# Performance work log

Hardware: AMD Instinct MI355X
Metric: run time of the kernel (lower is better)

Reference implementation:

```python
import jax, jax.numpy as jnp
import numpy as np

# Irreps config: node = 64x0e + 32x1o, edge sh = 1x0e + 1x1o
N, E = 50000, 800000
MUL0, MUL1 = 64, 32
D_IN = MUL0 + 3 * MUL1          # 160
FC_H = 64
W_NUMEL = MUL0 + MUL0 + MUL1 + MUL1  # 192, per-instruction uvu weights
SQRT3 = 1.7320508075688772
ACT_C = 1.6791   # e3nn normalize2mom constant for silu


def setup_inputs() -> dict:
    key = jax.random.key(0)
    ks = jax.random.split(key, 11)
    return {
        "x": jax.random.normal(ks[0], (N, D_IN), jnp.float32),
        "edge_scalars": jax.random.uniform(ks[1], (E, FC_H), dtype=jnp.float32),
        "edge_attr_sh": jax.random.normal(ks[2], (E, 4), jnp.float32),
        "edge_index": jax.random.randint(ks[3], (2, E), 0, N),
        "w_fc1": jax.random.normal(ks[4], (FC_H, FC_H), jnp.float32),
        "w_fc2": jax.random.normal(ks[5], (FC_H, W_NUMEL), jnp.float32),
        "w_sc_s": jax.random.normal(ks[6], (MUL0, MUL0), jnp.float32),
        "w_sc_v": jax.random.normal(ks[7], (MUL1, MUL1), jnp.float32),
        "w_lin_s": jax.random.normal(ks[8], (96, MUL0), jnp.float32),
        "w_lin_v": jax.random.normal(ks[9], (96, MUL1), jnp.float32),
        "w_alpha": jax.random.normal(ks[10], (96, 1), jnp.float32) * 0.1,
    }


def reference(x, edge_scalars, edge_attr_sh, edge_index, w_fc1, w_fc2,
              w_sc_s, w_sc_v, w_lin_s, w_lin_v, w_alpha):
    src, dst = edge_index[0], edge_index[1]

    # --- fc: FullyConnectedNet([64, 64, 192], silu), e3nn fan-in norm ---
    h = jax.nn.silu(edge_scalars @ w_fc1 / np.sqrt(FC_H)) * ACT_C
    weight = h @ w_fc2 / np.sqrt(FC_H)                       # [E, 192]
    w0 = weight[:, :MUL0]                 # 0e x 0e -> 0e (mul 64)
    w1 = weight[:, MUL0:2 * MUL0]         # 0e x 1o -> 1o (mul 64)
    w2 = weight[:, 2 * MUL0:2 * MUL0 + MUL1]   # 1o x 0e -> 1o (mul 32)
    w3 = weight[:, 2 * MUL0 + MUL1:]           # 1o x 1o -> 0e (mul 32)

    # --- self connection: o3.Linear(in -> out), per-irrep mixing ---
    x_s = x[:, :MUL0]                                   # [N, 64]
    x_v = x[:, MUL0:].reshape(N, MUL1, 3)               # [N, 32, 3]
    sc_s = x_s @ w_sc_s / np.sqrt(MUL0)
    sc_v = jnp.einsum('nui,uw->nwi', x_v, w_sc_v) / np.sqrt(MUL1)
    sc_out = jnp.concatenate([sc_s, sc_v.reshape(N, 3 * MUL1)], axis=1)

    # --- gather + edge-weighted uvu tensor product ---
    gx_s = x_s[src]                                     # [E, 64]
    gx_v = x_v[src]                                     # [E, 32, 3]
    sh_s = edge_attr_sh[:, 0:1]                         # [E, 1]
    sh_v = edge_attr_sh[:, 1:4]                         # [E, 3]

    # path weights fold with w3j so factors cancel for 1o outputs
    mid_s0 = w0 * gx_s * sh_s                                        # [E,64] 0e
    mid_s1 = w3 * jnp.einsum('eui,ei->eu', gx_v, sh_v) / SQRT3       # [E,32] 0e
    mid_v0 = w1[:, :, None] * gx_s[:, :, None] * sh_v[:, None, :]    # [E,64,3] 1o
    mid_v1 = w2[:, :, None] * gx_v * sh_s[:, :, None]                # [E,32,3] 1o
    edge_feat = jnp.concatenate(
        [mid_s0, mid_s1, mid_v0.reshape(E, 3 * MUL0), mid_v1.reshape(E, 3 * MUL1)],
        axis=1)                                                      # [E, 384]

    # --- scatter-mean to destination nodes ---
    seg = jax.ops.segment_sum(edge_feat, dst, num_segments=N)
    cnt = jax.ops.segment_sum(jnp.ones((E,), edge_feat.dtype), dst, num_segments=N)
    mean = seg / jnp.maximum(cnt, 1.0)[:, None]                      # [N, 384]

    m_s = mean[:, :96]                                   # 96x0e
    m_v = mean[:, 96:].reshape(N, 96, 3)                 # 96x1o

    # --- alpha gate (o3.Linear mid -> 0e) and output linear ---
    alpha = m_s @ w_alpha / np.sqrt(96)                  # [N, 1]
    lin_s = m_s @ w_lin_s / np.sqrt(96)                  # [N, 64]
    lin_v = jnp.einsum('nui,uw->nwi', m_v, w_lin_v) / np.sqrt(96)
    lin_out = jnp.concatenate([lin_s, lin_v.reshape(N, 3 * MUL1)], axis=1)

    # sc.output_mask is all-ones here (every output irrep reachable)
    return sc_out + alpha * lin_out
```

## Files before the change

### kernel.cpp

```cpp
#include <hip/hip_runtime.h>
#include <hip/hip_bf16.h>

#define N_NODES 50000
#define N_EDGES 800000
#define MUL0 64
#define MUL1 32
#define D_IN 160
#define FC_H 64
#define W_NUMEL 192
#define FEAT 384
#define ACT_C 1.6791f
#define INV_SQRT3 0.57735026918962576f
#define RSQRT32 0.17677669529663687f
#define RSQRT96 0.10206207261596575f

#define TILE 64

typedef __attribute__((ext_vector_type(8))) short s16x8;
typedef __attribute__((ext_vector_type(4))) float f32x4;
typedef _Float16 h8 __attribute__((ext_vector_type(8)));
typedef __fp16 fp16x2 __attribute__((ext_vector_type(2)));

static __device__ __forceinline__ unsigned short f2bf(float f) {
    __hip_bfloat16 b = __float2bfloat16(f);
    return __builtin_bit_cast(unsigned short, b);
}

static __device__ __forceinline__ int swz(int row, int byte_in_row) {
    return row * 128 + ((((byte_in_row >> 4) ^ (row & 7)) << 4) | (byte_in_row & 15));
}
static __device__ __forceinline__ h8 rdh8(const unsigned char* base, int row, int eb) {
    return *(const h8*)(base + swz(row, eb));
}


__global__ __launch_bounds__(256) void hist_kernel(const int* __restrict__ eidx,
                                                   int* __restrict__ cnt) {
    int e = blockIdx.x * 256 + threadIdx.x;
    if (e < N_EDGES) atomicAdd(&cnt[eidx[N_EDGES + e]], 1);
}

#define SCAN_NB 64
#define SCAN_CH ((N_NODES + SCAN_NB - 1) / SCAN_NB)

__global__ __launch_bounds__(256) void scanA_kernel(const int* __restrict__ cnt,
                                                    int* __restrict__ bsum) {
    __shared__ int sred[4];
    int b = blockIdx.x, t = threadIdx.x;
    int lim = min((b + 1) * SCAN_CH, N_NODES);
    int s = 0;
    for (int i = b * SCAN_CH + t; i < lim; i += 256) s += cnt[i];
    for (int d = 1; d < 64; d <<= 1) s += __shfl_xor(s, d);
    if ((t & 63) == 0) sred[t >> 6] = s;
    __syncthreads();
    if (t == 0) bsum[b] = sred[0] + sred[1] + sred[2] + sred[3];
}

__global__ __launch_bounds__(64) void scanB_kernel(const int* __restrict__ bsum,
                                                   int* __restrict__ boff) {
    int t = threadIdx.x;
    int v = bsum[t];
    int p = v;
    for (int d = 1; d < 64; d <<= 1) { int u = __shfl_up(p, d); if (t >= d) p += u; }
    boff[t] = p - v;
}

__global__ __launch_bounds__(256) void scanC_kernel(const int* __restrict__ cnt,
                                                    const int* __restrict__ boff,
                                                    int* __restrict__ fill) {
    __shared__ int s_w[4];
    int b = blockIdx.x, t = threadIdx.x;
    const int CH2 = (SCAN_CH + 255) / 256;
    int base = b * SCAN_CH + t * CH2;
    int lim = min((b + 1) * SCAN_CH, N_NODES);
    int s = 0;
#pragma unroll
    for (int k = 0; k < CH2; ++k) { int i = base + k; if (i < lim) s += cnt[i]; }
    int v = s;
    for (int d = 1; d < 64; d <<= 1) { int u = __shfl_up(v, d); if ((t & 63) >= d) v += u; }
    if ((t & 63) == 63) s_w[t >> 6] = v;
    __syncthreads();
    if (t == 0) { int run = 0; for (int w = 0; w < 4; ++w) { int tv = s_w[w]; s_w[w] = run; run += tv; } }
    __syncthreads();
    int run = boff[b] + s_w[t >> 6] + (v - s);
#pragma unroll
    for (int k = 0; k < CH2; ++k) {
        int i = base + k;
        if (i < lim) { fill[i] = run; run += cnt[i]; }
    }
}

__global__ __launch_bounds__(256) void scatter_ids_kernel(const int* __restrict__ eidx,
                                                          int* __restrict__ fill,
                                                          int* __restrict__ sorted_eid) {
    int e = blockIdx.x * 256 + threadIdx.x;
    if (e < N_EDGES) {
        int p = atomicAdd(&fill[eidx[N_EDGES + e]], 1);
        sorted_eid[p] = e;
    }
}

__global__ __launch_bounds__(256) void prep_w_kernel(
    const float* __restrict__ w_fc1,
    const float* __restrict__ w_fc2,
    const float* __restrict__ w_sc_s,
    const float* __restrict__ w_sc_v,
    const float* __restrict__ w_lin_s,
    const float* __restrict__ w_lin_v,
    unsigned short* __restrict__ w1t,
    unsigned short* __restrict__ w2t,
    unsigned short* __restrict__ wscs_t,
    unsigned short* __restrict__ wscv_t,
    unsigned short* __restrict__ wlins_t,
    unsigned short* __restrict__ wlinv_t)
{
    int i = blockIdx.x * 256 + threadIdx.x;
    if (i < 64 * 64)  w1t[i]    = f2bf(w_fc1[(i & 63) * FC_H + (i >> 6)]);
    if (i < 192 * 64) w2t[i]    = f2bf(w_fc2[(i & 63) * W_NUMEL + (i >> 6)]);
    if (i < 64 * 64)  wscs_t[i] = f2bf(w_sc_s[(i & 63) * 64 + (i >> 6)]);
    if (i < 32 * 32)  wscv_t[i] = f2bf(w_sc_v[(i & 31) * 32 + (i >> 5)]);
    if (i < 64 * 96)  wlins_t[i] = f2bf(w_lin_s[(i % 96) * 64 + (i / 96)]);
    if (i < 32 * 96)  wlinv_t[i] = f2bf(w_lin_v[(i % 96) * 32 + (i / 96)]);
}

#define X_OFF    0
#define W_OFF    20480
#define SH_OFF   45056
#define SID_OFF  45568
#define SEGN_OFF 45696
#define NSEG_OFF 45952
#define SMEM_SZ  45968

static __device__ __forceinline__ h8 seg_mask(const unsigned* vv, unsigned tgt) {
    h8 a;
#pragma unroll
    for (int w2 = 0; w2 < 4; ++w2) {
        a[w2 * 2]     = ((vv[w2] & 0xffffu) == tgt) ? (_Float16)1.f : (_Float16)0.f;
        a[w2 * 2 + 1] = ((vv[w2] >> 16)     == tgt) ? (_Float16)1.f : (_Float16)0.f;
    }
    return a;
}

__global__ __launch_bounds__(256) void edge_kernel(
    const float* __restrict__ x,
    const float* __restrict__ es,
    const float* __restrict__ sh,
    const int*   __restrict__ eidx,
    const int*   __restrict__ sorted_eid,
    const unsigned short* __restrict__ w1t,
    const unsigned short* __restrict__ w2t,
    float* __restrict__ accg)
{
    __shared__ __align__(16) unsigned char smem[SMEM_SZ];
    int* s_segnode = (int*)(smem + SEGN_OFF);
    unsigned short* s_sid = (unsigned short*)(smem + SID_OFF);

    const int t = threadIdx.x;
    const int l = t & 63;
    const int wv = t >> 6;
    const int lr = l & 15;
    const int lk = l >> 4;
    const int tile0 = blockIdx.x * TILE;

    int eid_own = sorted_eid[tile0 + wv * 16 + lr];
    float4 esf[4];
    {
        const float4* ep = (const float4*)(es + (size_t)eid_own * FC_H);
        esf[0] = ep[lk * 2];     esf[1] = ep[lk * 2 + 1];
        esf[2] = ep[8 + lk * 2]; esf[3] = ep[8 + lk * 2 + 1];
    }
    float4 xg[10];
    int xE[10], xC[10];
#pragma unroll
    for (int q = 0; q < 10; ++q) {
        int i = q * 256 + t;
        int e = i / 40, c4 = i - e * 40;
        xE[q] = e; xC[q] = c4;
        const float4* xp = (const float4*)(x + (size_t)eidx[sorted_eid[tile0 + e]] * D_IN);
        xg[q] = xp[c4];
    }
    float shv = sh[(size_t)sorted_eid[tile0 + (t >> 2)] * 4 + (t & 3)];
    if (wv == 0) {
        int dl = eidx[N_EDGES + sorted_eid[tile0 + l]];
        int nd = __shfl_down(dl, 1);
        bool flag = (l == 63) || (dl != nd);
        unsigned long long m = __ballot(flag);
        int sid = __popcll(m & ((1ull << l) - 1ull));
        s_sid[l] = (unsigned short)sid;
        if (flag) s_segnode[sid] = dl;
        if (l == 63) *(int*)(smem + NSEG_OFF) = sid + 1;
    }

    unsigned short* s_h = (unsigned short*)(smem + X_OFF);
    s16x8 afrag[2];
    {
        s16x8 a;
        a[0] = f2bf(esf[0].x); a[1] = f2bf(esf[0].y); a[2] = f2bf(esf[0].z); a[3] = f2bf(esf[0].w);
        a[4] = f2bf(esf[1].x); a[5] = f2bf(esf[1].y); a[6] = f2bf(esf[1].z); a[7] = f2bf(esf[1].w);
        afrag[0] = a;
        a[0] = f2bf(esf[2].x); a[1] = f2bf(esf[2].y); a[2] = f2bf(esf[2].z); a[3] = f2bf(esf[2].w);
        a[4] = f2bf(esf[3].x); a[5] = f2bf(esf[3].y); a[6] = f2bf(esf[3].z); a[7] = f2bf(esf[3].w);
        afrag[1] = a;
    }
#pragma unroll
    for (int nt = 0; nt < 4; ++nt) {
        f32x4 hacc = {0.f, 0.f, 0.f, 0.f};
#pragma unroll
        for (int kk = 0; kk < 2; ++kk) {
            s16x8 b = *(const s16x8*)(w1t + (nt * 16 + lr) * 64 + kk * 32 + lk * 8);
            hacc = __builtin_amdgcn_mfma_f32_16x16x32_bf16(afrag[kk], b, hacc, 0, 0, 0);
        }
#pragma unroll
        for (int q = 0; q < 4; ++q) {
            float aa = hacc[q] * 0.125f;
            float hv = aa * (1.f / (1.f + __expf(-aa))) * ACT_C;
            s_h[(wv * 16 + lk * 4 + q) * 72 + nt * 16 + lr] = f2bf(hv);
        }
    }
    s16x8 hfrag[2];
#pragma unroll
    for (int kk = 0; kk < 2; ++kk)
        hfrag[kk] = *(const s16x8*)(s_h + (wv * 16 + lr) * 72 + kk * 32 + lk * 8);
    __syncthreads();

#pragma unroll
    for (int nt = 0; nt < 12; ++nt) {
        f32x4 acc = {0.f, 0.f, 0.f, 0.f};
#pragma unroll
        for (int kk = 0; kk < 2; ++kk) {
            s16x8 b = *(const s16x8*)(w2t + (nt * 16 + lr) * 64 + kk * 32 + lk * 8);
            acc = __builtin_amdgcn_mfma_f32_16x16x32_bf16(hfrag[kk], b, acc, 0, 0, 0);
        }
        int f = nt * 16 + lr;
        fp16x2 p0 = __builtin_amdgcn_cvt_pkrtz(acc[0] * 0.125f, acc[1] * 0.125f);
        fp16x2 p1 = __builtin_amdgcn_cvt_pkrtz(acc[2] * 0.125f, acc[3] * 0.125f);
        uint2 wval = { __builtin_bit_cast(unsigned, p0), __builtin_bit_cast(unsigned, p1) };
        *(uint2*)(smem + W_OFF + swz(f, wv * 32 + lk * 8)) = wval;
    }
#pragma unroll
    for (int q = 0; q < 10; ++q) {
        float4 v = xg[q];
#pragma unroll
        for (int jj = 0; jj < 4; ++jj) {
            int r = xC[q] * 4 + jj;
            float fv = (jj == 0) ? v.x : (jj == 1) ? v.y : (jj == 2) ? v.z : v.w;
            *(_Float16*)(smem + X_OFF + swz(r, xE[q] * 2)) = (_Float16)fv;
        }
    }
    {
        int e = t >> 2, c = t & 3;
        *(_Float16*)(smem + SH_OFF + swz(c, e * 2)) = (_Float16)shv;
    }
    __syncthreads();

    const int nseg = *(const int*)(smem + NSEG_OFF);

    h8 shreg[4][2];
#pragma unroll
    for (int r = 0; r < 4; ++r)
#pragma unroll
        for (int ks = 0; ks < 2; ++ks)
            shreg[r][ks] = rdh8(smem + SH_OFF, r, ks * 64 + lk * 16);
    unsigned vv[2][4];
#pragma unroll
    for (int ks = 0; ks < 2; ++ks) {
        uint4 sv = *(const uint4*)(smem + SID_OFF + ks * 64 + lk * 16);
        vv[ks][0] = sv.x; vv[ks][1] = sv.y; vv[ks][2] = sv.z; vv[ks][3] = sv.w;
    }

    h8 Bv[4][2];
    int fcol[4];
    bool cls3j[4] = {false, false, false, false};
#pragma unroll
    for (int ks = 0; ks < 2; ++ks) {
        const int eb = ks * 64 + lk * 16;
        if (wv == 0) {
#pragma unroll
            for (int jj = 0; jj < 4; ++jj) {
                int col = jj * 16 + lr;
                Bv[jj][ks] = rdh8(smem + W_OFF, col, eb) * rdh8(smem + X_OFF, col, eb);
                fcol[jj] = col;
            }
        } else if (wv == 1) {
#pragma unroll
            for (int jj = 0; jj < 4; ++jj) {
                int col = jj * 16 + lr;
                Bv[jj][ks] = rdh8(smem + W_OFF, 128 + col / 3, eb) * rdh8(smem + X_OFF, 64 + col, eb);
                fcol[jj] = 288 + col;
            }
        } else if (wv == 2) {
#pragma unroll
            for (int jj = 0; jj < 2; ++jj) {
                int col = 64 + jj * 16 + lr;
                Bv[jj][ks] = rdh8(smem + W_OFF, 128 + col / 3, eb) * rdh8(smem + X_OFF, 64 + col, eb);
                fcol[jj] = 288 + col;
            }
#pragma unroll
            for (int jj = 2; jj < 4; ++jj) {
                int col = (jj - 2) * 16 + lr;
                h8 d = rdh8(smem + X_OFF, 64 + 3 * col, eb)     * shreg[1][ks]
                     + rdh8(smem + X_OFF, 64 + 3 * col + 1, eb) * shreg[2][ks]
                     + rdh8(smem + X_OFF, 64 + 3 * col + 2, eb) * shreg[3][ks];
                Bv[jj][ks] = rdh8(smem + W_OFF, 160 + col, eb) * d;
                fcol[jj] = 64 + col;
                cls3j[jj] = true;
            }
        } else {
#pragma unroll
            for (int jj = 0; jj < 4; ++jj) {
                int col = jj * 16 + lr;
                Bv[jj][ks] = rdh8(smem + W_OFF, 64 + col, eb) * rdh8(smem + X_OFF, col, eb);
                fcol[jj] = 96 + 3 * col;
            }
        }
    }

    if (wv != 3) {
        const int npass = (nseg + 15) >> 4;
        for (int p = 0; p < npass; ++p) {
            h8 bm0 = seg_mask(vv[0], (unsigned)(p * 16 + lr));
            h8 bm1 = seg_mask(vv[1], (unsigned)(p * 16 + lr));
            h8 As0 = bm0 * shreg[0][0];
            h8 As1 = bm1 * shreg[0][1];
            const int m0 = p * 16 + lk * 4;
            float* nptr[4]; bool valid[4], atq[4];
#pragma unroll
            for (int q = 0; q < 4; ++q) {
                int sg = m0 + q;
                valid[q] = sg < nseg;
                int node = valid[q] ? s_segnode[sg] : 0;
                nptr[q] = accg + (size_t)node * FEAT;
                atq[q] = (sg == 0) || (sg == nseg - 1);
            }
#pragma unroll
            for (int jj = 0; jj < 4; ++jj) {
                f32x4 acc = {0.f, 0.f, 0.f, 0.f};
                acc = __builtin_amdgcn_mfma_f32_16x16x32_f16(cls3j[jj] ? bm0 : As0, Bv[jj][0], acc, 0, 0, 0);
                acc = __builtin_amdgcn_mfma_f32_16x16x32_f16(cls3j[jj] ? bm1 : As1, Bv[jj][1], acc, 0, 0, 0);
                const float sc = cls3j[jj] ? INV_SQRT3 : 1.f;
#pragma unroll
                for (int q = 0; q < 4; ++q) {
                    if (valid[q]) {
                        float v = acc[q] * sc;
                        float* a = nptr[q] + fcol[jj];
                        if (atq[q]) atomicAdd(a, v); else *a = v;
                    }
                }
            }
        }
    } else {
        const int npass = (3 * nseg + 15) >> 4;
        for (int p = 0; p < npass; ++p) {
            int m = p * 16 + lr;
            int sgA = m / 3, i3A = m - 3 * sgA;
            h8 mk0 = seg_mask(vv[0], (unsigned)sgA);
            h8 mk1 = seg_mask(vv[1], (unsigned)sgA);
            h8 A0 = mk0 * ((i3A == 0) ? shreg[1][0] : (i3A == 1) ? shreg[2][0] : shreg[3][0]);
            h8 A1 = mk1 * ((i3A == 0) ? shreg[1][1] : (i3A == 1) ? shreg[2][1] : shreg[3][1]);
            int m0 = p * 16 + lk * 4;
            int sgq = m0 / 3, rq = m0 - 3 * sgq;
            float* nptr[4]; int i3q[4]; bool valid[4], atq[4];
#pragma unroll
            for (int q = 0; q < 4; ++q) {
                valid[q] = sgq < nseg;
                int node = valid[q] ? s_segnode[sgq] : 0;
                nptr[q] = accg + (size_t)node * FEAT;
                i3q[q] = rq;
                atq[q] = (sgq == 0) || (sgq == nseg - 1);
                if (++rq == 3) { rq = 0; ++sgq; }
            }
#pragma unroll
            for (int jj = 0; jj < 4; ++jj) {
                f32x4 acc = {0.f, 0.f, 0.f, 0.f};
                acc = __builtin_amdgcn_mfma_f32_16x16x32_f16(A0, Bv[jj][0], acc, 0, 0, 0);
                acc = __builtin_amdgcn_mfma_f32_16x16x32_f16(A1, Bv[jj][1], acc, 0, 0, 0);
#pragma unroll
                for (int q = 0; q < 4; ++q) {
                    if (valid[q]) {
                        float* a = nptr[q] + fcol[jj] + i3q[q];
                        if (atq[q]) atomicAdd(a, acc[q]); else *a = acc[q];
                    }
                }
            }
        }
    }
}


static __device__ __forceinline__ s16x8 frag_c8(const float* p, float s) {
    float4 u = *(const float4*)p, v = *(const float4*)(p + 4);
    s16x8 a;
    a[0] = f2bf(u.x * s); a[1] = f2bf(u.y * s); a[2] = f2bf(u.z * s); a[3] = f2bf(u.w * s);
    a[4] = f2bf(v.x * s); a[5] = f2bf(v.y * s); a[6] = f2bf(v.z * s); a[7] = f2bf(v.w * s);
    return a;
}

__global__ __launch_bounds__(256) void node_kernel(
    const float* __restrict__ x,
    const float* __restrict__ accg,
    const int*   __restrict__ cnt,
    const unsigned short* __restrict__ wscs_t,
    const unsigned short* __restrict__ wscv_t,
    const unsigned short* __restrict__ wlins_t,
    const unsigned short* __restrict__ wlinv_t,
    const float* __restrict__ w_alpha,
    float* __restrict__ out)
{
    const int t = threadIdx.x;
    const int wv = t >> 6, l = t & 63;
    const int lr = l & 15, lk = l >> 4;
    const int n_base = blockIdx.x * 64 + wv * 16;
    const int nrow = n_base + lr;
    const int nclamp = min(nrow, N_NODES - 1);

    const float* mrow = accg + (size_t)nclamp * FEAT;
    const float* xrow = x + (size_t)nclamp * D_IN;
    const float rinv = 1.f / (float)max(cnt[nclamp], 1);

    s16x8 ax[2], ams[3], axv[3], amv[3][3];
#pragma unroll
    for (int kk = 0; kk < 2; ++kk) ax[kk] = frag_c8(xrow + kk * 32 + lk * 8, 1.f);
#pragma unroll
    for (int kk = 0; kk < 3; ++kk) ams[kk] = frag_c8(mrow + kk * 32 + lk * 8, rinv);
    {
        float xb[24];
        const float4* p = (const float4*)(xrow + 64 + 24 * lk);
#pragma unroll
        for (int q = 0; q < 6; ++q) ((float4*)xb)[q] = p[q];
#pragma unroll
        for (int i = 0; i < 3; ++i) {
            s16x8 a;
#pragma unroll
            for (int j = 0; j < 8; ++j) a[j] = f2bf(xb[3 * j + i]);
            axv[i] = a;
        }
    }
#pragma unroll
    for (int kk = 0; kk < 3; ++kk) {
        float mb[24];
        const float4* p = (const float4*)(mrow + 96 + 96 * kk + 24 * lk);
#pragma unroll
        for (int q = 0; q < 6; ++q) ((float4*)mb)[q] = p[q];
#pragma unroll
        for (int i = 0; i < 3; ++i) {
            s16x8 a;
#pragma unroll
            for (int j = 0; j < 8; ++j) a[j] = f2bf(mb[3 * j + i] * rinv);
            amv[i][kk] = a;
        }
    }

    float ap = 0.f;
    {
        float ab[24];
        const float4* p = (const float4*)(mrow + 24 * lk);
#pragma unroll
        for (int q = 0; q < 6; ++q) ((float4*)ab)[q] = p[q];
#pragma unroll
        for (int j = 0; j < 24; ++j) ap += ab[j] * rinv * w_alpha[lk * 24 + j];
    }
    ap += __shfl_xor(ap, 16);
    ap += __shfl_xor(ap, 32);
    const float alphav = ap * RSQRT96;

    f32x4 accA[4], accL[4];
#pragma unroll
    for (int nt = 0; nt < 4; ++nt) { accA[nt] = (f32x4){0,0,0,0}; accL[nt] = (f32x4){0,0,0,0}; }
#pragma unroll
    for (int nt = 0; nt < 4; ++nt) {
#pragma unroll
        for (int kk = 0; kk < 2; ++kk) {
            s16x8 b = *(const s16x8*)(wscs_t + (nt * 16 + lr) * 64 + kk * 32 + lk * 8);
            accA[nt] = __builtin_amdgcn_mfma_f32_16x16x32_bf16(ax[kk], b, accA[nt], 0, 0, 0);
        }
#pragma unroll
        for (int kk = 0; kk < 3; ++kk) {
            s16x8 b = *(const s16x8*)(wlins_t + (nt * 16 + lr) * 96 + kk * 32 + lk * 8);
            accL[nt] = __builtin_amdgcn_mfma_f32_16x16x32_bf16(ams[kk], b, accL[nt], 0, 0, 0);
        }
    }
    f32x4 accVs[3][2], accVl[3][2];
#pragma unroll
    for (int i = 0; i < 3; ++i)
#pragma unroll
        for (int nt = 0; nt < 2; ++nt) { accVs[i][nt] = (f32x4){0,0,0,0}; accVl[i][nt] = (f32x4){0,0,0,0}; }
#pragma unroll
    for (int i = 0; i < 3; ++i) {
#pragma unroll
        for (int nt = 0; nt < 2; ++nt) {
            s16x8 b = *(const s16x8*)(wscv_t + (nt * 16 + lr) * 32 + lk * 8);
            accVs[i][nt] = __builtin_amdgcn_mfma_f32_16x16x32_bf16(axv[i], b, accVs[i][nt], 0, 0, 0);
#pragma unroll
            for (int kk = 0; kk < 3; ++kk) {
                s16x8 b2 = *(const s16x8*)(wlinv_t + (nt * 16 + lr) * 96 + kk * 32 + lk * 8);
                accVl[i][nt] = __builtin_amdgcn_mfma_f32_16x16x32_bf16(amv[i][kk], b2, accVl[i][nt], 0, 0, 0);
            }
        }
    }

#pragma unroll
    for (int q = 0; q < 4; ++q) {
        int row = lk * 4 + q;
        float ar = __shfl(alphav, row);
        int n = n_base + row;
        bool ok = (n < N_NODES);
        float* orow = out + (size_t)n * 160;
#pragma unroll
        for (int nt = 0; nt < 4; ++nt) {
            float vout = accA[nt][q] * 0.125f + ar * accL[nt][q] * RSQRT96;
            if (ok) orow[nt * 16 + lr] = vout;
        }
#pragma unroll
        for (int i = 0; i < 3; ++i)
#pragma unroll
            for (int nt = 0; nt < 2; ++nt) {
                float vout = accVs[i][nt][q] * RSQRT32 + ar * accVl[i][nt][q] * RSQRT96;
                if (ok) orow[64 + 3 * (nt * 16 + lr) + i] = vout;
            }
    }
}


extern "C" void kernel_launch(void* const* d_in, const int* in_sizes, int n_in,
                              void* d_out, int out_size, void* d_ws, size_t ws_size,
                              hipStream_t stream) {
    const float* x        = (const float*)d_in[0];
    const float* es       = (const float*)d_in[1];
    const float* sh       = (const float*)d_in[2];
    const int*   eidx     = (const int*)d_in[3];
    const float* w_fc1    = (const float*)d_in[4];
    const float* w_fc2    = (const float*)d_in[5];
    const float* w_sc_s   = (const float*)d_in[6];
    const float* w_sc_v   = (const float*)d_in[7];
    const float* w_lin_s  = (const float*)d_in[8];
    const float* w_lin_v  = (const float*)d_in[9];
    const float* w_alpha  = (const float*)d_in[10];
    float* out = (float*)d_out;

    float* accg       = (float*)d_ws;
    int*   cnt        = (int*)(accg + (size_t)N_NODES * FEAT);
    int*   fill       = cnt + N_NODES;
    int*   sorted_eid = fill + N_NODES;
    unsigned short* w1t     = (unsigned short*)(sorted_eid + N_EDGES);
    unsigned short* w2t     = w1t + 64 * 64;
    unsigned short* wscs_t  = w2t + 192 * 64;
    unsigned short* wscv_t  = wscs_t + 64 * 64;
    unsigned short* wlins_t = wscv_t + 32 * 32;
    unsigned short* wlinv_t = wlins_t + 64 * 96;
    int* bsum = (int*)(wlinv_t + 32 * 96);
    int* boff = bsum + SCAN_NB;

    (void)hipMemsetAsync(d_ws, 0, ((size_t)N_NODES * FEAT + N_NODES) * 4, stream);
    hipLaunchKernelGGL(hist_kernel, dim3((N_EDGES + 255) / 256), dim3(256), 0, stream,
                       eidx, cnt);
    hipLaunchKernelGGL(scanA_kernel, dim3(SCAN_NB), dim3(256), 0, stream, cnt, bsum);
    hipLaunchKernelGGL(scanB_kernel, dim3(1), dim3(64), 0, stream, bsum, boff);
    hipLaunchKernelGGL(scanC_kernel, dim3(SCAN_NB), dim3(256), 0, stream, cnt, boff, fill);
    hipLaunchKernelGGL(scatter_ids_kernel, dim3((N_EDGES + 255) / 256), dim3(256), 0, stream,
                       eidx, fill, sorted_eid);
    hipLaunchKernelGGL(prep_w_kernel, dim3(48), dim3(256), 0, stream,
                       w_fc1, w_fc2, w_sc_s, w_sc_v, w_lin_s, w_lin_v,
                       w1t, w2t, wscs_t, wscv_t, wlins_t, wlinv_t);
    hipLaunchKernelGGL(edge_kernel, dim3(N_EDGES / TILE), dim3(256), 0, stream,
                       x, es, sh, eidx, sorted_eid, w1t, w2t, accg);
    hipLaunchKernelGGL(node_kernel, dim3((N_NODES + 63) / 64), dim3(256), 0, stream,
                       x, accg, cnt, wscs_t, wscv_t, wlins_t, wlinv_t, w_alpha, out);
}
```

Measured before the change: 453.0 us.

## Split shared-memory tiles into per-half-edge slabs and coalesce node-feature gathers

Changes the swizzle so each 128-byte row holds two logical 64-byte rows, and splits the W, X and SH shared buffers into two slabs, one per 32-edge half. The node-feature gather changes so each thread loads ten contiguous float4s of a single source node instead of striding across edges, which removes the per-element div/mod indexing. The goal is better global coalescing per node row and fewer LDS bank conflicts on the half-precision transposed writes. It risks layout mismatches with the unseen consumers of these buffers, and it may raise register pressure.

```diff
diff --git a/kernel.cpp b/kernel.cpp
--- a/kernel.cpp
+++ b/kernel.cpp
@@ -27,7 +27,9 @@
 }
 
 static __device__ __forceinline__ int swz(int row, int byte_in_row) {
-    return row * 128 + ((((byte_in_row >> 4) ^ (row & 7)) << 4) | (byte_in_row & 15));
+    int unit = ((row & 1) << 2) | (byte_in_row >> 4);
+    int su = unit ^ ((row >> 1) & 7);
+    return (row >> 1) * 128 + su * 16 + (byte_in_row & 15);
 }
 static __device__ __forceinline__ h8 rdh8(const unsigned char* base, int row, int eb) {
     return *(const h8*)(base + swz(row, eb));
@@ -169,15 +171,15 @@
         esf[0] = ep[lk * 2];     esf[1] = ep[lk * 2 + 1];
         esf[2] = ep[8 + lk * 2]; esf[3] = ep[8 + lk * 2 + 1];
     }
+    const int hs   = t >> 7;
+    const int tt_h = t & 127;
+    const int xe   = tt_h & 31;
+    const int cgrp = tt_h >> 5;
     float4 xg[10];
-    int xE[10], xC[10];
-#pragma unroll
-    for (int q = 0; q < 10; ++q) {
-        int i = q * 256 + t;
-        int e = i / 40, c4 = i - e * 40;
-        xE[q] = e; xC[q] = c4;
-        const float4* xp = (const float4*)(x + (size_t)eidx[sorted_eid[tile0 + e]] * D_IN);
-        xg[q] = xp[c4];
+    {
+        const float4* xp = (const float4*)(x + (size_t)eidx[sorted_eid[tile0 + hs * 32 + xe]] * D_IN);
+#pragma unroll
+        for (int k = 0; k < 10; ++k) xg[k] = xp[cgrp * 10 + k];
     }
     float shv = sh[(size_t)sorted_eid[tile0 + (t >> 2)] * 4 + (t & 3)];
     if (wv == 0) {
@@ -223,47 +225,54 @@
         hfrag[kk] = *(const s16x8*)(s_h + (wv * 16 + lr) * 72 + kk * 32 + lk * 8);
     __syncthreads();
 
-#pragma unroll
-    for (int nt = 0; nt < 12; ++nt) {
-        f32x4 acc = {0.f, 0.f, 0.f, 0.f};
-#pragma unroll
-        for (int kk = 0; kk < 2; ++kk) {
-            s16x8 b = *(const s16x8*)(w2t + (nt * 16 + lr) * 64 + kk * 32 + lk * 8);
-            acc = __builtin_amdgcn_mfma_f32_16x16x32_bf16(hfrag[kk], b, acc, 0, 0, 0);
-        }
-        int f = nt * 16 + lr;
-        fp16x2 p0 = __builtin_amdgcn_cvt_pkrtz(acc[0] * 0.125f, acc[1] * 0.125f);
-        fp16x2 p1 = __builtin_amdgcn_cvt_pkrtz(acc[2] * 0.125f, acc[3] * 0.125f);
-        uint2 wval = { __builtin_bit_cast(unsigned, p0), __builtin_bit_cast(unsigned, p1) };
-        *(uint2*)(smem + W_OFF + swz(f, wv * 32 + lk * 8)) = wval;
-    }
-#pragma unroll
-    for (int q = 0; q < 10; ++q) {
-        float4 v = xg[q];
-#pragma unroll
-        for (int jj = 0; jj < 4; ++jj) {
-            int r = xC[q] * 4 + jj;
-            float fv = (jj == 0) ? v.x : (jj == 1) ? v.y : (jj == 2) ? v.z : v.w;
-            *(_Float16*)(smem + X_OFF + swz(r, xE[q] * 2)) = (_Float16)fv;
+    {
+        const int ws = wv >> 1;
+        const int ebyte = (wv & 1) * 32 + lk * 8;
+        unsigned char* bw = smem + W_OFF + ws * 12288;
+#pragma unroll
+        for (int nt = 0; nt < 12; ++nt) {
+            f32x4 acc = {0.f, 0.f, 0.f, 0.f};
+#pragma unroll
+            for (int kk = 0; kk < 2; ++kk) {
+                s16x8 b = *(const s16x8*)(w2t + (nt * 16 + lr) * 64 + kk * 32 + lk * 8);
+                acc = __builtin_amdgcn_mfma_f32_16x16x32_bf16(hfrag[kk], b, acc, 0, 0, 0);
+            }
+            int f = nt * 16 + lr;
+            fp16x2 p0 = __builtin_amdgcn_cvt_pkrtz(acc[0] * 0.125f, acc[1] * 0.125f);
+            fp16x2 p1 = __builtin_amdgcn_cvt_pkrtz(acc[2] * 0.125f, acc[3] * 0.125f);
+            uint2 wval = { __builtin_bit_cast(unsigned, p0), __builtin_bit_cast(unsigned, p1) };
+            *(uint2*)(bw + swz(f, ebyte)) = wval;
+        }
+    }
+    {
+        unsigned char* bx = smem + X_OFF + hs * 10240;
+#pragma unroll
+        for (int k = 0; k < 10; ++k) {
+            float4 v = xg[k];
+#pragma unroll
+            for (int jj = 0; jj < 4; ++jj) {
+                int r = (cgrp * 10 + k) * 4 + jj;
+                float fv = (jj == 0) ? v.x : (jj == 1) ? v.y : (jj == 2) ? v.z : v.w;
+                *(_Float16*)(bx + swz(r, xe * 2)) = (_Float16)fv;
+            }
         }
     }
     {
         int e = t >> 2, c = t & 3;
-        *(_Float16*)(smem + SH_OFF + swz(c, e * 2)) = (_Float16)shv;
+        *(_Float16*)(smem + SH_OFF + (e >> 5) * 256 + swz(c, (e & 31) * 2)) = (_Float16)shv;
     }
     __syncthreads();
 
     const int nseg = *(const int*)(smem + NSEG_OFF);
+    const int eb = lk * 16;
 
     h8 shreg[4][2];
-#pragma unroll
-    for (int r = 0; r < 4; ++r)
-#pragma unroll
-        for (int ks = 0; ks < 2; ++ks)
-            shreg[r][ks] = rdh8(smem + SH_OFF, r, ks * 64 + lk * 16);
     unsigned vv[2][4];
 #pragma unroll
     for (int ks = 0; ks < 2; ++ks) {
+#pragma unroll
+        for (int r = 0; r < 4; ++r)
+            shreg[r][ks] = rdh8(smem + SH_OFF + ks * 256, r, eb);
         uint4 sv = *(const uint4*)(smem + SID_OFF + ks * 64 + lk * 16);
         vv[ks][0] = sv.x; vv[ks][1] = sv.y; vv[ks][2] = sv.z; vv[ks][3] = sv.w;
     }
@@ -273,35 +282,36 @@
     bool cls3j[4] = {false, false, false, false};
 #pragma unroll
     for (int ks = 0; ks < 2; ++ks) {
-        const int eb = ks * 64 + lk * 16;
+        const unsigned char* bx = smem + X_OFF + ks * 10240;
+        const unsigned char* bw = smem + W_OFF + ks * 12288;
         if (wv == 0) {
 #pragma unroll
             for (int jj = 0; jj < 4; ++jj) {
                 int col = jj * 16 + lr;
-                Bv[jj][ks] = rdh8(smem + W_OFF, col, eb) * rdh8(smem + X_OFF, col, eb);
+                Bv[jj][ks] = rdh8(bw, col, eb) * rdh8(bx, col, eb);
                 fcol[jj] = col;
             }
         } else if (wv == 1) {
 #pragma unroll
             for (int jj = 0; jj < 4; ++jj) {
                 int col = jj * 16 + lr;
-                Bv[jj][ks] = rdh8(smem + W_OFF, 128 + col / 3, eb) * rdh8(smem + X_OFF, 64 + col, eb);
+                Bv[jj][ks] = rdh8(bw, 128 + col / 3, eb) * rdh8(bx, 64 + col, eb);
                 fcol[jj] = 288 + col;
             }
         } else if (wv == 2) {
 #pragma unroll
             for (int jj = 0; jj < 2; ++jj) {
                 int col = 64 + jj * 16 + lr;
-                Bv[jj][ks] = rdh8(smem + W_OFF, 128 + col / 3, eb) * rdh8(smem + X_OFF, 64 + col, eb);
+                Bv[jj][ks] = rdh8(bw, 128 + col / 3, eb) * rdh8(bx, 64 + col, eb);
                 fcol[jj] = 288 + col;
             }
 #pragma unroll
             for (int jj = 2; jj < 4; ++jj) {
                 int col = (jj - 2) * 16 + lr;
-                h8 d = rdh8(smem + X_OFF, 64 + 3 * col, eb)     * shreg[1][ks]
-                     + rdh8(smem + X_OFF, 64 + 3 * col + 1, eb) * shreg[2][ks]
-                     + rdh8(smem + X_OFF, 64 + 3 * col + 2, eb) * shreg[3][ks];
-                Bv[jj][ks] = rdh8(smem + W_OFF, 160 + col, eb) * d;
+                h8 d = rdh8(bx, 64 + 3 * col, eb)     * shreg[1][ks]
+                     + rdh8(bx, 64 + 3 * col + 1, eb) * shreg[2][ks]
+                     + rdh8(bx, 64 + 3 * col + 2, eb) * shreg[3][ks];
+                Bv[jj][ks] = rdh8(bw, 160 + col, eb) * d;
                 fcol[jj] = 64 + col;
                 cls3j[jj] = true;
             }
@@ -309,7 +319,7 @@
 #pragma unroll
             for (int jj = 0; jj < 4; ++jj) {
                 int col = jj * 16 + lr;
-                Bv[jj][ks] = rdh8(smem + W_OFF, 64 + col, eb) * rdh8(smem + X_OFF, col, eb);
+                Bv[jj][ks] = rdh8(bw, 64 + col, eb) * rdh8(bx, col, eb);
                 fcol[jj] = 96 + 3 * col;
             }
         }
```

New measurement: 453.6 us. About the same (+0.1%).
